# Optimization experiments

Hardware: AMD Instinct MI355X
Metric: run time of the kernel (lower is better)

Reference implementation:

```python
import jax, jax.numpy as jnp
import numpy as np

EPS_W = 1e-8   # weight reciprocal eps (matches torch code)
EPS_BN = 1e-5  # torch BatchNorm1d default eps


def _cdist(a, b):
    # a: [B,N,3], b: [B,M,3] -> [B,N,M] euclidean distances
    sq = (jnp.sum(a * a, -1)[:, :, None] + jnp.sum(b * b, -1)[:, None, :]
          - 2.0 * jnp.einsum('bnd,bmd->bnm', a, b))
    return jnp.sqrt(jnp.maximum(sq, 0.0))


def _bn_relu(x, gamma, beta):
    # x: [B,C,N]; training-mode batch norm over (B,N)
    mean = jnp.mean(x, axis=(0, 2), keepdims=True)
    var = jnp.mean((x - mean) ** 2, axis=(0, 2), keepdims=True)
    y = (x - mean) * jax.lax.rsqrt(var + EPS_BN)
    y = y * gamma[None, :, None] + beta[None, :, None]
    return jax.nn.relu(y)


def setup_inputs() -> dict:
    key = jax.random.key(0)
    ks = jax.random.split(key, 8)
    B, Np, Ns = 16, 1024, 4096
    Cp, Cs, Co = 256, 128, 256
    return {
        'xyz_prev': jax.random.normal(ks[0], (B, Np, 3), jnp.float32),
        'xyz_skip': jax.random.normal(ks[1], (B, Ns, 3), jnp.float32),
        'points_prev': jax.random.normal(ks[2], (B, Cp, Np), jnp.float32),
        'points_skip': jax.random.normal(ks[3], (B, Cs, Ns), jnp.float32),
        'W1': jax.random.normal(ks[4], (Co, Cp + Cs), jnp.float32) * 0.05,
        'g1': jnp.ones((Co,), jnp.float32),
        'b1': jnp.zeros((Co,), jnp.float32),
        'W2': jax.random.normal(ks[5], (Co, Co), jnp.float32) * 0.05,
        'g2': jnp.ones((Co,), jnp.float32),
        'b2': jnp.zeros((Co,), jnp.float32),
    }


def reference(xyz_prev, xyz_skip, points_prev, points_skip, W1, g1, b1, W2, g2, b2):
    dist = _cdist(xyz_skip, xyz_prev)                       # [B,Ns,Np]
    neg, idx = jax.lax.top_k(-dist, 3)                      # 3 smallest dists
    dist_recip = 1.0 / (dist + EPS_W)
    # NOTE: normalization is over ALL N_prev points (faithful to source)
    weight = dist_recip / jnp.sum(dist_recip, axis=2, keepdims=True)
    w3 = jnp.take_along_axis(weight, idx, axis=2)           # [B,Ns,3]
    pp = jnp.swapaxes(points_prev, 1, 2)                    # [B,Np,Cp]
    g = jnp.take_along_axis(pp[:, None, :, :], idx[..., None], axis=2)  # [B,Ns,3,Cp]
    interp = jnp.einsum('bnk,bnkc->bcn', w3, g)             # [B,Cp,Ns]
    x = jnp.concatenate([interp, points_skip], axis=1)      # [B,Cp+Cs,Ns]
    x = _bn_relu(jnp.einsum('bcn,oc->bon', x, W1), g1, b1)
    x = _bn_relu(jnp.einsum('bcn,oc->bon', x, W2), g2, b2)
    return x
```

## Files before the change

### kernel.cpp

```cpp
#include <hip/hip_runtime.h>
#include <math.h>

constexpr int NB  = 16;
constexpr int NP  = 1024;
constexpr int NS  = 4096;
constexpr int CP  = 256;
constexpr int CS  = 128;
constexpr int CIN = 384;
constexpr int CO  = 256;

constexpr int NCHUNK = 8;
constexpr int CHPTS  = NP / NCHUNK;

typedef unsigned int uint;
typedef unsigned short ushort_t;
typedef __attribute__((ext_vector_type(8))) short short8;
typedef __attribute__((ext_vector_type(4))) float f32x4;

__device__ __forceinline__ ushort_t f2bf(float f) {
  uint u = __float_as_uint(f);
  uint r = (u + 0x7fffu + ((u >> 16) & 1u)) >> 16;
  return (ushort_t)r;
}
__device__ __forceinline__ float bf2f(ushort_t u) {
  return __uint_as_float(((uint)u) << 16);
}
__device__ __forceinline__ uint pk2(ushort_t lo, ushort_t hi) {
  return (uint)lo | ((uint)hi << 16);
}

__device__ __forceinline__ void gload16(const void* g, void* l) {
  __builtin_amdgcn_global_load_lds(
      (const __attribute__((address_space(1))) uint*)g,
      (__attribute__((address_space(3))) uint*)l, 16, 0, 0);
}

__device__ __forceinline__ void tk_step(float pxv, float pyv, float pzv, int pi,
                                        float qx, float qy, float qz,
                                        float& d0, float& d1, float& d2,
                                        int& i0, int& i1, int& i2, float& rsum) {
  float dx = pxv - qx, dy = pyv - qy, dz = pzv - qz;
  float sq = fmaf(dz, dz, fmaf(dy, dy, fmaf(dx, dx, 1e-16f)));
  rsum += __builtin_amdgcn_rsqf(sq);
  bool c0 = sq < d0, c1 = sq < d1, c2 = sq < d2;
  i2 = c2 ? (c1 ? i1 : pi) : i2;
  i1 = c1 ? (c0 ? i0 : pi) : i1;
  i0 = c0 ? pi : i0;
  d2 = __builtin_amdgcn_fmed3f(d1, d2, sq);
  d1 = __builtin_amdgcn_fmed3f(d0, d1, sq);
  d0 = fminf(d0, sq);
}

__global__ __launch_bounds__(256) void topk_chunk_kernel(
    const float* __restrict__ xyz_prev, const float* __restrict__ xyz_skip,
    float* __restrict__ pbuf) {
  __shared__ float px[CHPTS], py[CHPTS], pz[CHPTS];
  int q  = blockIdx.y;
  int b  = blockIdx.z;
  int tid = threadIdx.x;
  if (tid < CHPTS) {
    const float* xp = xyz_prev + ((size_t)b * NP + q * CHPTS + tid) * 3;
    px[tid] = xp[0]; py[tid] = xp[1]; pz[tid] = xp[2];
  }
  __syncthreads();
  int nA = blockIdx.x * 512 + tid;
  int nB = nA + 256;
  const float* xqA = xyz_skip + ((size_t)b * NS + nA) * 3;
  const float* xqB = xyz_skip + ((size_t)b * NS + nB) * 3;
  float qxA = xqA[0], qyA = xqA[1], qzA = xqA[2];
  float qxB = xqB[0], qyB = xqB[1], qzB = xqB[2];
  float dA0 = INFINITY, dA1 = INFINITY, dA2 = INFINITY;
  float dB0 = INFINITY, dB1 = INFINITY, dB2 = INFINITY;
  int iA0 = -1, iA1 = -1, iA2 = -1, iB0 = -1, iB1 = -1, iB2 = -1;
  float rsA = 0.f, rsB = 0.f;
  int pbase = q * CHPTS;

  for (int p = 0; p < CHPTS; p += 4) {
    float4 X = *(const float4*)&px[p];
    float4 Y = *(const float4*)&py[p];
    float4 Z = *(const float4*)&pz[p];
    tk_step(X.x, Y.x, Z.x, pbase + p + 0, qxA, qyA, qzA, dA0, dA1, dA2, iA0, iA1, iA2, rsA);
    tk_step(X.x, Y.x, Z.x, pbase + p + 0, qxB, qyB, qzB, dB0, dB1, dB2, iB0, iB1, iB2, rsB);
    tk_step(X.y, Y.y, Z.y, pbase + p + 1, qxA, qyA, qzA, dA0, dA1, dA2, iA0, iA1, iA2, rsA);
    tk_step(X.y, Y.y, Z.y, pbase + p + 1, qxB, qyB, qzB, dB0, dB1, dB2, iB0, iB1, iB2, rsB);
    tk_step(X.z, Y.z, Z.z, pbase + p + 2, qxA, qyA, qzA, dA0, dA1, dA2, iA0, iA1, iA2, rsA);
    tk_step(X.z, Y.z, Z.z, pbase + p + 2, qxB, qyB, qzB, dB0, dB1, dB2, iB0, iB1, iB2, rsB);
    tk_step(X.w, Y.w, Z.w, pbase + p + 3, qxA, qyA, qzA, dA0, dA1, dA2, iA0, iA1, iA2, rsA);
    tk_step(X.w, Y.w, Z.w, pbase + p + 3, qxB, qyB, qzB, dB0, dB1, dB2, iB0, iB1, iB2, rsB);
  }

  size_t PA = ((size_t)(b * NCHUNK + q) * NS + nA) * 8;
  size_t PB = ((size_t)(b * NCHUNK + q) * NS + nB) * 8;
  float4 a0 = make_float4(dA0, dA1, dA2, rsA);
  float4 a1; a1.x = __int_as_float(iA0); a1.y = __int_as_float(iA1);
  a1.z = __int_as_float(iA2); a1.w = 0.f;
  float4 b0 = make_float4(dB0, dB1, dB2, rsB);
  float4 b1; b1.x = __int_as_float(iB0); b1.y = __int_as_float(iB1);
  b1.z = __int_as_float(iB2); b1.w = 0.f;
  *(float4*)(pbuf + PA) = a0;
  *(float4*)(pbuf + PA + 4) = a1;
  *(float4*)(pbuf + PB) = b0;
  *(float4*)(pbuf + PB + 4) = b1;
}

__global__ __launch_bounds__(256) void topk_merge_kernel(
    const float* __restrict__ pbuf, float* __restrict__ w3,
    int* __restrict__ idx3) {
  int gid = blockIdx.x * 256 + threadIdx.x;
  int b = gid >> 12;
  int n = gid & (NS - 1);
  float d0 = INFINITY, d1 = INFINITY, d2 = INFINITY;
  int i0 = -1, i1 = -1, i2 = -1;
  float rsum = 0.f;
  for (int q = 0; q < NCHUNK; q++) {
    size_t P = ((size_t)(b * NCHUNK + q) * NS + n) * 8;
    float4 v0 = *(const float4*)(pbuf + P);
    float4 v1 = *(const float4*)(pbuf + P + 4);
    rsum += v0.w;
    float ds[3] = {v0.x, v0.y, v0.z};
    int   is[3] = {__float_as_int(v1.x), __float_as_int(v1.y),
                   __float_as_int(v1.z)};
    #pragma unroll
    for (int k = 0; k < 3; k++) {
      float sq = ds[k]; int pi = is[k];
      bool c0 = sq < d0, c1 = sq < d1, c2 = sq < d2;
      i2 = c2 ? (c1 ? i1 : pi) : i2;
      i1 = c1 ? (c0 ? i0 : pi) : i1;
      i0 = c0 ? pi : i0;
      d2 = __builtin_amdgcn_fmed3f(d1, d2, sq);
      d1 = __builtin_amdgcn_fmed3f(d0, d1, sq);
      d0 = fminf(d0, sq);
    }
  }
  float inv = 1.0f / rsum;
  size_t base = (size_t)gid * 3;
  w3[base + 0] = __builtin_amdgcn_rsqf(d0) * inv;
  w3[base + 1] = __builtin_amdgcn_rsqf(d1) * inv;
  w3[base + 2] = __builtin_amdgcn_rsqf(d2) * inv;
  idx3[base + 0] = i0; idx3[base + 1] = i1; idx3[base + 2] = i2;
}

__global__ __launch_bounds__(256) void wcast_kernel(
    const float* __restrict__ W1, const float* __restrict__ W2,
    ushort_t* __restrict__ W1b, ushort_t* __restrict__ W2b,
    float* __restrict__ st1, float* __restrict__ st2) {
  int tid = threadIdx.x;
  if (blockIdx.x == 0) {
    st1[tid] = 0.f; st1[tid + 256] = 0.f;
    st2[tid] = 0.f; st2[tid + 256] = 0.f;
  }
  int t = blockIdx.x * 256 + tid;
  int n1 = CO * CIN / 4;
  if (t < n1) {
    float4 v = *(const float4*)(W1 + t * 4);
    ushort4 o; o.x = f2bf(v.x); o.y = f2bf(v.y); o.z = f2bf(v.z); o.w = f2bf(v.w);
    *(ushort4*)(W1b + t * 4) = o;
  } else {
    int u = t - n1;
    float4 v = *(const float4*)(W2 + u * 4);
    ushort4 o; o.x = f2bf(v.x); o.y = f2bf(v.y); o.z = f2bf(v.z); o.w = f2bf(v.w);
    *(ushort4*)(W2b + u * 4) = o;
  }
}

__global__ __launch_bounds__(256) void ppT_kernel(
    const float* __restrict__ pp, ushort_t* __restrict__ pptT) {
  __shared__ float tl[64][65];
  int p0 = blockIdx.x * 64, c0 = blockIdx.y * 64, b = blockIdx.z;
  int tid = threadIdx.x;
  const float* P = pp + (size_t)b * CP * NP;
  int pi4 = (tid & 15) * 4, ci = tid >> 4;
  #pragma unroll
  for (int r = 0; r < 4; r++) {
    int cc = ci + 16 * r;
    float4 v = *(const float4*)(P + (size_t)(c0 + cc) * NP + p0 + pi4);
    tl[cc][pi4] = v.x; tl[cc][pi4 + 1] = v.y; tl[cc][pi4 + 2] = v.z; tl[cc][pi4 + 3] = v.w;
  }
  __syncthreads();
  ushort_t* O = pptT + (size_t)b * NP * CP;
  int ci4 = (tid & 15) * 4, pi = tid >> 4;
  #pragma unroll
  for (int r = 0; r < 4; r++) {
    int pr = pi + 16 * r;
    ushort4 o;
    o.x = f2bf(tl[ci4 + 0][pr]); o.y = f2bf(tl[ci4 + 1][pr]);
    o.z = f2bf(tl[ci4 + 2][pr]); o.w = f2bf(tl[ci4 + 3][pr]);
    *(ushort4*)(O + (size_t)(p0 + pr) * CP + c0 + ci4) = o;
  }
}

__global__ __launch_bounds__(256) void skipT_kernel(
    const float* __restrict__ sk, ushort_t* __restrict__ x1) {
  __shared__ float tl[64][65];
  int n0 = blockIdx.x * 64, c0 = blockIdx.y * 64, b = blockIdx.z;
  int tid = threadIdx.x;
  const float* S = sk + (size_t)b * CS * NS;
  int ni4 = (tid & 15) * 4, ci = tid >> 4;
  #pragma unroll
  for (int r = 0; r < 4; r++) {
    int cc = ci + 16 * r;
    float4 v = *(const float4*)(S + (size_t)(c0 + cc) * NS + n0 + ni4);
    tl[cc][ni4] = v.x; tl[cc][ni4 + 1] = v.y; tl[cc][ni4 + 2] = v.z; tl[cc][ni4 + 3] = v.w;
  }
  __syncthreads();
  ushort_t* O = x1 + (size_t)b * NS * CIN;
  int ci4 = (tid & 15) * 4, ni = tid >> 4;
  #pragma unroll
  for (int r = 0; r < 4; r++) {
    int nr = ni + 16 * r;
    ushort4 o;
    o.x = f2bf(tl[ci4 + 0][nr]); o.y = f2bf(tl[ci4 + 1][nr]);
    o.z = f2bf(tl[ci4 + 2][nr]); o.w = f2bf(tl[ci4 + 3][nr]);
    *(ushort4*)(O + (size_t)(n0 + nr) * CIN + CP + c0 + ci4) = o;
  }
}

__global__ __launch_bounds__(256) void interp_kernel(
    const ushort_t* __restrict__ pptT, const float* __restrict__ w3,
    const int* __restrict__ idx3, ushort_t* __restrict__ x1) {
  int tid = threadIdx.x;
  int nl = tid >> 6, l = tid & 63;
  int b = blockIdx.y;
  int n = blockIdx.x * 4 + nl;
  size_t nb = (size_t)b * NS + n;
  int j0 = idx3[nb * 3 + 0], j1 = idx3[nb * 3 + 1], j2 = idx3[nb * 3 + 2];
  float w0 = w3[nb * 3 + 0], w1 = w3[nb * 3 + 1], w2 = w3[nb * 3 + 2];
  const ushort_t* P = pptT + (size_t)b * NP * CP;
  int c = l * 4;
  ushort4 g0 = *(const ushort4*)(P + (size_t)j0 * CP + c);
  ushort4 g1 = *(const ushort4*)(P + (size_t)j1 * CP + c);
  ushort4 g2 = *(const ushort4*)(P + (size_t)j2 * CP + c);
  ushort4 o;
  o.x = f2bf(w0 * bf2f(g0.x) + w1 * bf2f(g1.x) + w2 * bf2f(g2.x));
  o.y = f2bf(w0 * bf2f(g0.y) + w1 * bf2f(g1.y) + w2 * bf2f(g2.y));
  o.z = f2bf(w0 * bf2f(g0.z) + w1 * bf2f(g1.z) + w2 * bf2f(g2.z));
  o.w = f2bf(w0 * bf2f(g0.w) + w1 * bf2f(g1.w) + w2 * bf2f(g2.w));
  *(ushort4*)(x1 + nb * CIN + c) = o;
}

template <int KD, bool ACT>
__global__ __launch_bounds__(256) void gemm_mfma_kernel(
    const ushort_t* __restrict__ X, const ushort_t* __restrict__ Wb,
    const float* __restrict__ aa, const float* __restrict__ ss,
    ushort_t* __restrict__ Yb, float* __restrict__ stats) {
  __shared__ ushort_t ldsX[128 * 32];
  __shared__ ushort_t ldsW[128 * 32];
  __shared__ float ssum[128], ssq[128];
  int tid = threadIdx.x;
  int w = tid >> 6, l = tid & 63;
  int n0 = blockIdx.x * 128;
  int by = blockIdx.y;
  int bz = blockIdx.z;
  if (tid < 128) { ssum[tid] = 0.f; ssq[tid] = 0.f; }

  f32x4 acc[4][4];
  #pragma unroll
  for (int i = 0; i < 4; i++)
    #pragma unroll
    for (int j = 0; j < 4; j++) acc[i][j] = {0.f, 0.f, 0.f, 0.f};

  int wn = (w & 1) * 64, wo = (w >> 1) * 64;
  int lr = l & 15, lk = l >> 4;
  const ushort_t* Xb = X + (size_t)bz * NS * KD;
  int rbase = w * 16 + (l >> 2);
  int cl = l & 3;
  int ksw = 8 * (cl ^ ((rbase >> 1) & 3));

  for (int kt = 0; kt < KD / 32; kt++) {
    int k0 = kt * 32;
    int ks = k0 + ksw;
    #pragma unroll
    for (int q = 0; q < 2; q++) {
      int r = q * 64 + rbase;
      gload16(Wb + (size_t)(by * 128 + r) * KD + ks, &ldsW[(q * 64 + w * 16) * 32]);
    }
    if constexpr (!ACT) {
      #pragma unroll
      for (int q = 0; q < 2; q++) {
        int r = q * 64 + rbase;
        gload16(Xb + (size_t)(n0 + r) * KD + ks, &ldsX[(q * 64 + w * 16) * 32]);
      }
    } else {
      float4 av0 = *(const float4*)(aa + ks);
      float4 av1 = *(const float4*)(aa + ks + 4);
      float4 sv0 = *(const float4*)(ss + ks);
      float4 sv1 = *(const float4*)(ss + ks + 4);
      #pragma unroll
      for (int q = 0; q < 2; q++) {
        int r = q * 64 + rbase;
        const ushort_t* src = Xb + (size_t)(n0 + r) * KD + ks;
        ushort4 v0 = *(const ushort4*)(src);
        ushort4 v1 = *(const ushort4*)(src + 4);
        int4 o;
        o.x = (int)pk2(f2bf(fmaxf(fmaf(av0.x, bf2f(v0.x), sv0.x), 0.f)),
                       f2bf(fmaxf(fmaf(av0.y, bf2f(v0.y), sv0.y), 0.f)));
        o.y = (int)pk2(f2bf(fmaxf(fmaf(av0.z, bf2f(v0.z), sv0.z), 0.f)),
                       f2bf(fmaxf(fmaf(av0.w, bf2f(v0.w), sv0.w), 0.f)));
        o.z = (int)pk2(f2bf(fmaxf(fmaf(av1.x, bf2f(v1.x), sv1.x), 0.f)),
                       f2bf(fmaxf(fmaf(av1.y, bf2f(v1.y), sv1.y), 0.f)));
        o.w = (int)pk2(f2bf(fmaxf(fmaf(av1.z, bf2f(v1.z), sv1.z), 0.f)),
                       f2bf(fmaxf(fmaf(av1.w, bf2f(v1.w), sv1.w), 0.f)));
        *(int4*)&ldsX[(q * 64 + w * 16) * 32 + l * 8] = o;
      }
    }
    __syncthreads();
    short8 a[4], bfr[4];
    #pragma unroll
    for (int i = 0; i < 4; i++) {
      int rr = wn + i * 16 + lr;
      int cs = lk ^ ((rr >> 1) & 3);
      a[i] = *(const short8*)&ldsX[rr * 32 + cs * 8];
    }
    #pragma unroll
    for (int j = 0; j < 4; j++) {
      int rr = wo + j * 16 + lr;
      int cs = lk ^ ((rr >> 1) & 3);
      bfr[j] = *(const short8*)&ldsW[rr * 32 + cs * 8];
    }
    #pragma unroll
    for (int i = 0; i < 4; i++)
      #pragma unroll
      for (int j = 0; j < 4; j++)
        acc[i][j] = __builtin_amdgcn_mfma_f32_16x16x32_bf16(a[i], bfr[j], acc[i][j], 0, 0, 0);
    __syncthreads();
  }

  #pragma unroll
  for (int j = 0; j < 4; j++) {
    int ol = wo + j * 16 + lr;
    int og = by * 128 + ol;
    float ps = 0.f, pq = 0.f;
    #pragma unroll
    for (int i = 0; i < 4; i++) {
      #pragma unroll
      for (int rg = 0; rg < 4; rg++) {
        float v = acc[i][j][rg];
        ps += v; pq += v * v;
        int n = n0 + wn + i * 16 + lk * 4 + rg;
        Yb[((size_t)bz * NS + n) * CO + og] = f2bf(v);
      }
    }
    atomicAdd(&ssum[ol], ps);
    atomicAdd(&ssq[ol], pq);
  }
  __syncthreads();
  if (tid < 128) {
    atomicAdd(&stats[by * 128 + tid], ssum[tid]);
    atomicAdd(&stats[CO + by * 128 + tid], ssq[tid]);
  }
}

__global__ void bnstats_kernel(const float* __restrict__ stats,
                               const float* __restrict__ g,
                               const float* __restrict__ bt,
                               float* __restrict__ a, float* __restrict__ s) {
  int o = threadIdx.x;
  float cnt = (float)NB * (float)NS;
  float m = stats[o] / cnt;
  float var = stats[CO + o] / cnt - m * m;
  var = fmaxf(var, 0.f);
  float inv = rsqrtf(var + 1e-5f);
  float av = g[o] * inv;
  a[o] = av; s[o] = bt[o] - m * av;
}

__global__ __launch_bounds__(256) void bnrelu_tr_kernel(
    const ushort_t* __restrict__ y2b, const float* __restrict__ a2,
    const float* __restrict__ s2, float* __restrict__ out) {
  __shared__ float tl[64][65];
  int n0 = blockIdx.x * 64, o0 = blockIdx.y * 64, b = blockIdx.z;
  const ushort_t* Y = y2b + (size_t)b * NS * CO;
  int tid = threadIdx.x;
  int o8 = (tid & 7) * 8, row = tid >> 3;
  #pragma unroll
  for (int r = 0; r < 2; r++) {
    int ii = row + 32 * r;
    const ushort_t* src = Y + (size_t)(n0 + ii) * CO + o0 + o8;
    ushort4 v0 = *(const ushort4*)(src);
    ushort4 v1 = *(const ushort4*)(src + 4);
    tl[ii][o8 + 0] = bf2f(v0.x); tl[ii][o8 + 1] = bf2f(v0.y);
    tl[ii][o8 + 2] = bf2f(v0.z); tl[ii][o8 + 3] = bf2f(v0.w);
    tl[ii][o8 + 4] = bf2f(v1.x); tl[ii][o8 + 5] = bf2f(v1.y);
    tl[ii][o8 + 6] = bf2f(v1.z); tl[ii][o8 + 7] = bf2f(v1.w);
  }
  __syncthreads();
  float* O = out + (size_t)b * CO * NS;
  int ii4 = (tid & 15) * 4, j = tid >> 4;
  #pragma unroll
  for (int r = 0; r < 4; r++) {
    int jj = j + 16 * r;
    float av = a2[o0 + jj], sv = s2[o0 + jj];
    float4 v;
    v.x = fmaxf(fmaf(av, tl[ii4 + 0][jj], sv), 0.f);
    v.y = fmaxf(fmaf(av, tl[ii4 + 1][jj], sv), 0.f);
    v.z = fmaxf(fmaf(av, tl[ii4 + 2][jj], sv), 0.f);
    v.w = fmaxf(fmaf(av, tl[ii4 + 3][jj], sv), 0.f);
    *(float4*)(O + (size_t)(o0 + jj) * NS + n0 + ii4) = v;
  }
}

extern "C" void kernel_launch(void* const* d_in, const int* in_sizes, int n_in,
                              void* d_out, int out_size, void* d_ws, size_t ws_size,
                              hipStream_t stream) {
  const float* xyz_prev    = (const float*)d_in[0];
  const float* xyz_skip    = (const float*)d_in[1];
  const float* points_prev = (const float*)d_in[2];
  const float* points_skip = (const float*)d_in[3];
  const float* W1 = (const float*)d_in[4];
  const float* g1 = (const float*)d_in[5];
  const float* b1 = (const float*)d_in[6];
  const float* W2 = (const float*)d_in[7];
  const float* g2 = (const float*)d_in[8];
  const float* b2 = (const float*)d_in[9];
  float* out = (float*)d_out;

  char* W = (char*)d_ws;
  size_t off = 0;
  auto alloc = [&](size_t bytes) {
    size_t o = off; off = (off + bytes + 255) & ~(size_t)255; return o;
  };
  ushort_t* x1   = (ushort_t*)(W + alloc((size_t)NB * NS * CIN * 2));
  ushort_t* y1b  = (ushort_t*)(W + alloc((size_t)NB * NS * CO * 2));
  ushort_t* pptT = (ushort_t*)(W + alloc((size_t)NB * NP * CP * 2));
  ushort_t* W1b  = (ushort_t*)(W + alloc((size_t)CO * CIN * 2));
  ushort_t* W2b  = (ushort_t*)(W + alloc((size_t)CO * CO * 2));
  float* w3   = (float*)(W + alloc((size_t)NB * NS * 3 * 4));
  int*   idx3 = (int*)(W + alloc((size_t)NB * NS * 3 * 4));
  float* st1  = (float*)(W + alloc(512 * 4));
  float* st2  = (float*)(W + alloc(512 * 4));
  float* ab   = (float*)(W + alloc(1024 * 4));
  float* a1 = ab, *s1 = ab + 256, *a2 = ab + 512, *s2 = ab + 768;
  size_t y2_off = alloc((size_t)NB * NS * CO * 2);
  bool full = (ws_size >= off);
  ushort_t* y2b = full ? (ushort_t*)(W + y2_off) : (ushort_t*)d_out;
  float* pbuf = full ? (float*)(W + y2_off) : (float*)d_out;

  hipLaunchKernelGGL(topk_chunk_kernel, dim3(NS / 512, NCHUNK, NB), dim3(256), 0,
                     stream, xyz_prev, xyz_skip, pbuf);
  hipLaunchKernelGGL(topk_merge_kernel, dim3(NB * NS / 256), dim3(256), 0, stream,
                     pbuf, w3, idx3);
  hipLaunchKernelGGL(wcast_kernel, dim3((CO * CIN / 4 + CO * CO / 4 + 255) / 256),
                     dim3(256), 0, stream, W1, W2, W1b, W2b, st1, st2);
  hipLaunchKernelGGL(ppT_kernel, dim3(NP / 64, CP / 64, NB), dim3(256), 0, stream,
                     points_prev, pptT);
  hipLaunchKernelGGL(skipT_kernel, dim3(NS / 64, CS / 64, NB), dim3(256), 0, stream,
                     points_skip, x1);
  hipLaunchKernelGGL(interp_kernel, dim3(NS / 4, NB), dim3(256), 0, stream,
                     pptT, w3, idx3, x1);
  hipLaunchKernelGGL((gemm_mfma_kernel<CIN, false>), dim3(NS / 128, 2, NB), dim3(256),
                     0, stream, x1, W1b, (const float*)nullptr, (const float*)nullptr,
                     y1b, st1);
  hipLaunchKernelGGL(bnstats_kernel, dim3(1), dim3(256), 0, stream, st1, g1, b1, a1, s1);
  hipLaunchKernelGGL((gemm_mfma_kernel<CO, true>), dim3(NS / 128, 2, NB), dim3(256),
                     0, stream, y1b, W2b, a1, s1, y2b, st2);
  hipLaunchKernelGGL(bnstats_kernel, dim3(1), dim3(256), 0, stream, st2, g2, b2, a2, s2);
  if (full) {
    hipLaunchKernelGGL(bnrelu_tr_kernel, dim3(NS / 64, CO / 64, NB), dim3(256), 0,
                       stream, y2b, a2, s2, out);
  } else {
    float* stage = (float*)d_ws;
    hipLaunchKernelGGL(bnrelu_tr_kernel, dim3(NS / 64, CO / 64, NB), dim3(256), 0,
                       stream, y2b, a2, s2, stage);
    hipMemcpyAsync(out, stage, (size_t)NB * NS * CO * 4, hipMemcpyDeviceToDevice,
                   stream);
  }
}
```

Before: 176.7 us.

## Pack neighbor index into distance bits, fuse BN stats into consumers

Top-3 search now packs the point index into the low 10 mantissa bits of the squared distance. Selection then uses only med3/min with no index selects, and the partial buffer shrinks to one float4 per query. The chunk count doubles for more parallelism. The separate BN statistics kernels are removed and their finalization is recomputed per block inside the second GEMM and the final bn-relu transpose kernel, and GEMM blocks are remapped on a 1D grid. Truncating the distance mantissa slightly perturbs weights and tie ordering.

```diff
diff --git a/kernel.cpp b/kernel.cpp
--- a/kernel.cpp
+++ b/kernel.cpp
@@ -9,7 +9,7 @@
 constexpr int CIN = 384;
 constexpr int CO  = 256;
 
-constexpr int NCHUNK = 8;
+constexpr int NCHUNK = 16;
 constexpr int CHPTS  = NP / NCHUNK;
 
 typedef unsigned int uint;
@@ -35,20 +35,17 @@
       (__attribute__((address_space(3))) uint*)l, 16, 0, 0);
 }
 
-__device__ __forceinline__ void tk_step(float pxv, float pyv, float pzv, int pi,
-                                        float qx, float qy, float qz,
-                                        float& d0, float& d1, float& d2,
-                                        int& i0, int& i1, int& i2, float& rsum) {
+__device__ __forceinline__ void tkp(float pxv, float pyv, float pzv, int pi,
+                                    float qx, float qy, float qz,
+                                    float& k0, float& k1, float& k2,
+                                    float& rsum) {
   float dx = pxv - qx, dy = pyv - qy, dz = pzv - qz;
   float sq = fmaf(dz, dz, fmaf(dy, dy, fmaf(dx, dx, 1e-16f)));
   rsum += __builtin_amdgcn_rsqf(sq);
-  bool c0 = sq < d0, c1 = sq < d1, c2 = sq < d2;
-  i2 = c2 ? (c1 ? i1 : pi) : i2;
-  i1 = c1 ? (c0 ? i0 : pi) : i1;
-  i0 = c0 ? pi : i0;
-  d2 = __builtin_amdgcn_fmed3f(d1, d2, sq);
-  d1 = __builtin_amdgcn_fmed3f(d0, d1, sq);
-  d0 = fminf(d0, sq);
+  float k = __uint_as_float((__float_as_uint(sq) & 0xFFFFFC00u) | (uint)pi);
+  k2 = __builtin_amdgcn_fmed3f(k1, k2, k);
+  k1 = __builtin_amdgcn_fmed3f(k0, k1, k);
+  k0 = fminf(k0, k);
 }
 
 __global__ __launch_bounds__(256) void topk_chunk_kernel(
@@ -69,9 +66,8 @@
   const float* xqB = xyz_skip + ((size_t)b * NS + nB) * 3;
   float qxA = xqA[0], qyA = xqA[1], qzA = xqA[2];
   float qxB = xqB[0], qyB = xqB[1], qzB = xqB[2];
-  float dA0 = INFINITY, dA1 = INFINITY, dA2 = INFINITY;
-  float dB0 = INFINITY, dB1 = INFINITY, dB2 = INFINITY;
-  int iA0 = -1, iA1 = -1, iA2 = -1, iB0 = -1, iB1 = -1, iB2 = -1;
+  float kA0 = INFINITY, kA1 = INFINITY, kA2 = INFINITY;
+  float kB0 = INFINITY, kB1 = INFINITY, kB2 = INFINITY;
   float rsA = 0.f, rsB = 0.f;
   int pbase = q * CHPTS;
 
@@ -79,28 +75,20 @@
     float4 X = *(const float4*)&px[p];
     float4 Y = *(const float4*)&py[p];
     float4 Z = *(const float4*)&pz[p];
-    tk_step(X.x, Y.x, Z.x, pbase + p + 0, qxA, qyA, qzA, dA0, dA1, dA2, iA0, iA1, iA2, rsA);
-    tk_step(X.x, Y.x, Z.x, pbase + p + 0, qxB, qyB, qzB, dB0, dB1, dB2, iB0, iB1, iB2, rsB);
-    tk_step(X.y, Y.y, Z.y, pbase + p + 1, qxA, qyA, qzA, dA0, dA1, dA2, iA0, iA1, iA2, rsA);
-    tk_step(X.y, Y.y, Z.y, pbase + p + 1, qxB, qyB, qzB, dB0, dB1, dB2, iB0, iB1, iB2, rsB);
-    tk_step(X.z, Y.z, Z.z, pbase + p + 2, qxA, qyA, qzA, dA0, dA1, dA2, iA0, iA1, iA2, rsA);
-    tk_step(X.z, Y.z, Z.z, pbase + p + 2, qxB, qyB, qzB, dB0, dB1, dB2, iB0, iB1, iB2, rsB);
-    tk_step(X.w, Y.w, Z.w, pbase + p + 3, qxA, qyA, qzA, dA0, dA1, dA2, iA0, iA1, iA2, rsA);
-    tk_step(X.w, Y.w, Z.w, pbase + p + 3, qxB, qyB, qzB, dB0, dB1, dB2, iB0, iB1, iB2, rsB);
-  }
-
-  size_t PA = ((size_t)(b * NCHUNK + q) * NS + nA) * 8;
-  size_t PB = ((size_t)(b * NCHUNK + q) * NS + nB) * 8;
-  float4 a0 = make_float4(dA0, dA1, dA2, rsA);
-  float4 a1; a1.x = __int_as_float(iA0); a1.y = __int_as_float(iA1);
-  a1.z = __int_as_float(iA2); a1.w = 0.f;
-  float4 b0 = make_float4(dB0, dB1, dB2, rsB);
-  float4 b1; b1.x = __int_as_float(iB0); b1.y = __int_as_float(iB1);
-  b1.z = __int_as_float(iB2); b1.w = 0.f;
-  *(float4*)(pbuf + PA) = a0;
-  *(float4*)(pbuf + PA + 4) = a1;
-  *(float4*)(pbuf + PB) = b0;
-  *(float4*)(pbuf + PB + 4) = b1;
+    tkp(X.x, Y.x, Z.x, pbase + p + 0, qxA, qyA, qzA, kA0, kA1, kA2, rsA);
+    tkp(X.x, Y.x, Z.x, pbase + p + 0, qxB, qyB, qzB, kB0, kB1, kB2, rsB);
+    tkp(X.y, Y.y, Z.y, pbase + p + 1, qxA, qyA, qzA, kA0, kA1, kA2, rsA);
+    tkp(X.y, Y.y, Z.y, pbase + p + 1, qxB, qyB, qzB, kB0, kB1, kB2, rsB);
+    tkp(X.z, Y.z, Z.z, pbase + p + 2, qxA, qyA, qzA, kA0, kA1, kA2, rsA);
+    tkp(X.z, Y.z, Z.z, pbase + p + 2, qxB, qyB, qzB, kB0, kB1, kB2, rsB);
+    tkp(X.w, Y.w, Z.w, pbase + p + 3, qxA, qyA, qzA, kA0, kA1, kA2, rsA);
+    tkp(X.w, Y.w, Z.w, pbase + p + 3, qxB, qyB, qzB, kB0, kB1, kB2, rsB);
+  }
+
+  size_t PA = ((size_t)(b * NCHUNK + q) * NS + nA) * 4;
+  size_t PB = ((size_t)(b * NCHUNK + q) * NS + nB) * 4;
+  *(float4*)(pbuf + PA) = make_float4(kA0, kA1, kA2, rsA);
+  *(float4*)(pbuf + PB) = make_float4(kB0, kB1, kB2, rsB);
 }
 
 __global__ __launch_bounds__(256) void topk_merge_kernel(
@@ -109,35 +97,34 @@
   int gid = blockIdx.x * 256 + threadIdx.x;
   int b = gid >> 12;
   int n = gid & (NS - 1);
-  float d0 = INFINITY, d1 = INFINITY, d2 = INFINITY;
-  int i0 = -1, i1 = -1, i2 = -1;
+  float k0 = INFINITY, k1 = INFINITY, k2 = INFINITY;
   float rsum = 0.f;
+  #pragma unroll 4
   for (int q = 0; q < NCHUNK; q++) {
-    size_t P = ((size_t)(b * NCHUNK + q) * NS + n) * 8;
-    float4 v0 = *(const float4*)(pbuf + P);
-    float4 v1 = *(const float4*)(pbuf + P + 4);
-    rsum += v0.w;
-    float ds[3] = {v0.x, v0.y, v0.z};
-    int   is[3] = {__float_as_int(v1.x), __float_as_int(v1.y),
-                   __float_as_int(v1.z)};
-    #pragma unroll
-    for (int k = 0; k < 3; k++) {
-      float sq = ds[k]; int pi = is[k];
-      bool c0 = sq < d0, c1 = sq < d1, c2 = sq < d2;
-      i2 = c2 ? (c1 ? i1 : pi) : i2;
-      i1 = c1 ? (c0 ? i0 : pi) : i1;
-      i0 = c0 ? pi : i0;
-      d2 = __builtin_amdgcn_fmed3f(d1, d2, sq);
-      d1 = __builtin_amdgcn_fmed3f(d0, d1, sq);
-      d0 = fminf(d0, sq);
-    }
+    float4 v = *(const float4*)(pbuf + ((size_t)(b * NCHUNK + q) * NS + n) * 4);
+    rsum += v.w;
+    k2 = __builtin_amdgcn_fmed3f(k1, k2, v.x);
+    k1 = __builtin_amdgcn_fmed3f(k0, k1, v.x);
+    k0 = fminf(k0, v.x);
+    k2 = __builtin_amdgcn_fmed3f(k1, k2, v.y);
+    k1 = __builtin_amdgcn_fmed3f(k0, k1, v.y);
+    k0 = fminf(k0, v.y);
+    k2 = __builtin_amdgcn_fmed3f(k1, k2, v.z);
+    k1 = __builtin_amdgcn_fmed3f(k0, k1, v.z);
+    k0 = fminf(k0, v.z);
   }
   float inv = 1.0f / rsum;
+  uint u0 = __float_as_uint(k0), u1 = __float_as_uint(k1), u2 = __float_as_uint(k2);
+  float d0 = __uint_as_float(u0 & 0xFFFFFC00u);
+  float d1 = __uint_as_float(u1 & 0xFFFFFC00u);
+  float d2 = __uint_as_float(u2 & 0xFFFFFC00u);
   size_t base = (size_t)gid * 3;
   w3[base + 0] = __builtin_amdgcn_rsqf(d0) * inv;
   w3[base + 1] = __builtin_amdgcn_rsqf(d1) * inv;
   w3[base + 2] = __builtin_amdgcn_rsqf(d2) * inv;
-  idx3[base + 0] = i0; idx3[base + 1] = i1; idx3[base + 2] = i2;
+  idx3[base + 0] = (int)(u0 & 1023u);
+  idx3[base + 1] = (int)(u1 & 1023u);
+  idx3[base + 2] = (int)(u2 & 1023u);
 }
 
 __global__ __launch_bounds__(256) void wcast_kernel(
@@ -241,17 +228,32 @@
 template <int KD, bool ACT>
 __global__ __launch_bounds__(256) void gemm_mfma_kernel(
     const ushort_t* __restrict__ X, const ushort_t* __restrict__ Wb,
-    const float* __restrict__ aa, const float* __restrict__ ss,
+    const float* __restrict__ stats_in, const float* __restrict__ g_in,
+    const float* __restrict__ bt_in,
     ushort_t* __restrict__ Yb, float* __restrict__ stats) {
   __shared__ ushort_t ldsX[128 * 32];
   __shared__ ushort_t ldsW[128 * 32];
   __shared__ float ssum[128], ssq[128];
+  __shared__ float a1s[ACT ? CO : 1], s1s[ACT ? CO : 1];
   int tid = threadIdx.x;
   int w = tid >> 6, l = tid & 63;
-  int n0 = blockIdx.x * 128;
-  int by = blockIdx.y;
-  int bz = blockIdx.z;
+  int bid = blockIdx.x;
+  int by = (bid >> 3) & 1;
+  int s  = (bid & 7) + 8 * (bid >> 4);
+  int bx = s & 31;
+  int bz = s >> 5;
+  int n0 = bx * 128;
   if (tid < 128) { ssum[tid] = 0.f; ssq[tid] = 0.f; }
+  if constexpr (ACT) {
+    float cnt = (float)NB * (float)NS;
+    float m = stats_in[tid] / cnt;
+    float var = stats_in[CO + tid] / cnt - m * m;
+    var = fmaxf(var, 0.f);
+    float invs = rsqrtf(var + 1e-5f);
+    float av = g_in[tid] * invs;
+    a1s[tid] = av; s1s[tid] = bt_in[tid] - m * av;
+  }
+  __syncthreads();
 
   f32x4 acc[4][4];
   #pragma unroll
@@ -281,10 +283,10 @@
         gload16(Xb + (size_t)(n0 + r) * KD + ks, &ldsX[(q * 64 + w * 16) * 32]);
       }
     } else {
-      float4 av0 = *(const float4*)(aa + ks);
-      float4 av1 = *(const float4*)(aa + ks + 4);
-      float4 sv0 = *(const float4*)(ss + ks);
-      float4 sv1 = *(const float4*)(ss + ks + 4);
+      float4 av0 = *(const float4*)&a1s[ks];
+      float4 av1 = *(const float4*)&a1s[ks + 4];
+      float4 sv0 = *(const float4*)&s1s[ks];
+      float4 sv1 = *(const float4*)&s1s[ks + 4];
       #pragma unroll
       for (int q = 0; q < 2; q++) {
         int r = q * 64 + rbase;
@@ -350,27 +352,25 @@
   }
 }
 
-__global__ void bnstats_kernel(const float* __restrict__ stats,
-                               const float* __restrict__ g,
-                               const float* __restrict__ bt,
-                               float* __restrict__ a, float* __restrict__ s) {
-  int o = threadIdx.x;
-  float cnt = (float)NB * (float)NS;
-  float m = stats[o] / cnt;
-  float var = stats[CO + o] / cnt - m * m;
-  var = fmaxf(var, 0.f);
-  float inv = rsqrtf(var + 1e-5f);
-  float av = g[o] * inv;
-  a[o] = av; s[o] = bt[o] - m * av;
-}
-
 __global__ __launch_bounds__(256) void bnrelu_tr_kernel(
-    const ushort_t* __restrict__ y2b, const float* __restrict__ a2,
-    const float* __restrict__ s2, float* __restrict__ out) {
+    const ushort_t* __restrict__ y2b, const float* __restrict__ stats_in,
+    const float* __restrict__ g_in, const float* __restrict__ bt_in,
+    float* __restrict__ out) {
   __shared__ float tl[64][65];
+  __shared__ float a2s[64], s2s[64];
   int n0 = blockIdx.x * 64, o0 = blockIdx.y * 64, b = blockIdx.z;
   const ushort_t* Y = y2b + (size_t)b * NS * CO;
   int tid = threadIdx.x;
+  if (tid < 64) {
+    int o = o0 + tid;
+    float cnt = (float)NB * (float)NS;
+    float m = stats_in[o] / cnt;
+    float var = stats_in[CO + o] / cnt - m * m;
+    var = fmaxf(var, 0.f);
+    float invs = rsqrtf(var + 1e-5f);
+    float av = g_in[o] * invs;
+    a2s[tid] = av; s2s[tid] = bt_in[o] - m * av;
+  }
   int o8 = (tid & 7) * 8, row = tid >> 3;
   #pragma unroll
   for (int r = 0; r < 2; r++) {
@@ -389,7 +389,7 @@
   #pragma unroll
   for (int r = 0; r < 4; r++) {
     int jj = j + 16 * r;
-    float av = a2[o0 + jj], sv = s2[o0 + jj];
+    float av = a2s[jj], sv = s2s[jj];
     float4 v;
     v.x = fmaxf(fmaf(av, tl[ii4 + 0][jj], sv), 0.f);
     v.y = fmaxf(fmaf(av, tl[ii4 + 1][jj], sv), 0.f);
@@ -428,8 +428,6 @@
   int*   idx3 = (int*)(W + alloc((size_t)NB * NS * 3 * 4));
   float* st1  = (float*)(W + alloc(512 * 4));
   float* st2  = (float*)(W + alloc(512 * 4));
-  float* ab   = (float*)(W + alloc(1024 * 4));
-  float* a1 = ab, *s1 = ab + 256, *a2 = ab + 512, *s2 = ab + 768;
   size_t y2_off = alloc((size_t)NB * NS * CO * 2);
   bool full = (ws_size >= off);
   ushort_t* y2b = full ? (ushort_t*)(W + y2_off) : (ushort_t*)d_out;
@@ -447,20 +445,18 @@
                      points_skip, x1);
   hipLaunchKernelGGL(interp_kernel, dim3(NS / 4, NB), dim3(256), 0, stream,
                      pptT, w3, idx3, x1);
-  hipLaunchKernelGGL((gemm_mfma_kernel<CIN, false>), dim3(NS / 128, 2, NB), dim3(256),
-                     0, stream, x1, W1b, (const float*)nullptr, (const float*)nullptr,
-                     y1b, st1);
-  hipLaunchKernelGGL(bnstats_kernel, dim3(1), dim3(256), 0, stream, st1, g1, b1, a1, s1);
-  hipLaunchKernelGGL((gemm_mfma_kernel<CO, true>), dim3(NS / 128, 2, NB), dim3(256),
-                     0, stream, y1b, W2b, a1, s1, y2b, st2);
-  hipLaunchKernelGGL(bnstats_kernel, dim3(1), dim3(256), 0, stream, st2, g2, b2, a2, s2);
+  hipLaunchKernelGGL((gemm_mfma_kernel<CIN, false>), dim3(1024), dim3(256),
+                     0, stream, x1, W1b, (const float*)nullptr,
+                     (const float*)nullptr, (const float*)nullptr, y1b, st1);
+  hipLaunchKernelGGL((gemm_mfma_kernel<CO, true>), dim3(1024), dim3(256),
+                     0, stream, y1b, W2b, st1, g1, b1, y2b, st2);
   if (full) {
     hipLaunchKernelGGL(bnrelu_tr_kernel, dim3(NS / 64, CO / 64, NB), dim3(256), 0,
-                       stream, y2b, a2, s2, out);
+                       stream, y2b, st2, g2, b2, out);
   } else {
     float* stage = (float*)d_ws;
     hipLaunchKernelGGL(bnrelu_tr_kernel, dim3(NS / 64, CO / 64, NB), dim3(256), 0,
-                       stream, y2b, a2, s2, stage);
+                       stream, y2b, st2, g2, b2, stage);
     hipMemcpyAsync(out, stage, (size_t)NB * NS * CO * 4, hipMemcpyDeviceToDevice,
                    stream);
   }
```

Measured after the change: 157.9 us. -10.6%, faster.
